# Kernel tuning notes

Hardware: AMD Instinct MI355X
Metric: run time of the kernel (lower is better)

Reference implementation:

```python
import jax, jax.numpy as jnp
import numpy as np

EPS = 1e-5
POOL_R, POOL_T, SCALE = 5, 7, 0.125  # pool_r, pool_t, 1/pool_stride


def conv_bn_relu(x, W, b, gamma, beta, pad):
    # Conv2d(bias) + BatchNorm2d (training-mode batch stats, biased var) + ReLU
    y = jax.lax.conv_general_dilated(x, W, (1, 1), [(pad, pad), (pad, pad)],
                                     dimension_numbers=('NCHW', 'OIHW', 'NCHW'))
    y = y + b[None, :, None, None]
    mean = y.mean(axis=(0, 2, 3))
    var = y.var(axis=(0, 2, 3))
    y = (y - mean[None, :, None, None]) * jax.lax.rsqrt(var + EPS)[None, :, None, None]
    y = y * gamma[None, :, None, None] + beta[None, :, None, None]
    return jax.nn.relu(y)


def linear_bn_relu(x, W, b, gamma, beta):
    # LinearBlock: Linear + BatchNorm (over batch dim) + ReLU
    y = x @ W.T + b
    mean = y.mean(axis=0)
    var = y.var(axis=0)
    y = (y - mean) * jax.lax.rsqrt(var + EPS) * gamma + beta
    return jax.nn.relu(y)


def _hat_int(x):
    # Antiderivative of the triangular (bilinear) hat kernel at offset x.
    u = jnp.clip(x, -1.0, 1.0)
    return jnp.where(u <= 0, 0.5 * (1.0 + u) ** 2, 0.5 + u - 0.5 * u ** 2)


def prroi_pool(feat, rois, ph, pw, scale):
    # Exact PrRoIPool2D. feat: [B,C,H,W]; rois: [B,N,4] xyxy in image coords.
    # Bilinear interp is a sum of separable hat kernels at integer grid points, so the
    # exact bin integral factorizes into per-axis hat-integral weights Wx, Wy.
    B, C, H, W = feat.shape
    x1, y1, x2, y2 = [rois[..., i] * scale for i in range(4)]
    bw = (x2 - x1) / pw   # [B,N]
    bh = (y2 - y1) / ph
    qx = jnp.arange(pw, dtype=feat.dtype)
    qy = jnp.arange(ph, dtype=feat.dtype)
    xs_lo = x1[..., None] + qx * bw[..., None]   # [B,N,Pw]
    ys_lo = y1[..., None] + qy * bh[..., None]   # [B,N,Ph]
    gw = jnp.arange(W, dtype=feat.dtype)
    gh = jnp.arange(H, dtype=feat.dtype)
    Wx = _hat_int(xs_lo[..., None] + bw[..., None, None] - gw) - _hat_int(xs_lo[..., None] - gw)  # [B,N,Pw,W]
    Wy = _hat_int(ys_lo[..., None] + bh[..., None, None] - gh) - _hat_int(ys_lo[..., None] - gh)  # [B,N,Ph,H]
    out = jnp.einsum('bchw,bnph,bnqw->bncpq', feat, Wy, Wx)
    area = (bw * bh)[:, :, None, None, None]
    return jnp.where(area > 0, out / jnp.maximum(area, 1e-12), 0.0)  # [B,N,C,Ph,Pw]


def _forward(feat1, feat2, bb1, proposals2,
             w_c1r, b_c1r, g_c1r, be_c1r,
             w_c1t, b_c1t, g_c1t, be_c1t,
             w_c2t, b_c2t, g_c2t, be_c2t,
             w_f1r, b_f1r, g_f1r, be_f1r,
             w_f2r, b_f2r, g_f2r, be_f2r,
             w_f1rt, b_f1rt, g_f1rt, be_f1rt,
             w_f2rt, b_f2rt, g_f2rt, be_f2rt,
             w_iou, b_iou):
    S = feat2.shape[0]
    N = proposals2.shape[2]
    # --- get_modulation ---
    c3_r = conv_bn_relu(feat1, w_c1r, b_c1r, g_c1r, be_c1r, 1)
    bb = bb1[0]  # [S,4] xywh -> xyxy
    roi_r = jnp.concatenate([bb[:, :2], bb[:, :2] + bb[:, 2:4]], axis=1)[:, None, :]
    pooled_r = prroi_pool(c3_r, roi_r, POOL_R, POOL_R, SCALE)[:, 0]   # [S,256,5,5]
    m = conv_bn_relu(pooled_r, w_f1r, b_f1r, g_f1r, be_f1r, 0)        # [S,1024,1,1]
    m = conv_bn_relu(m, w_f2r, b_f2r, g_f2r, be_f2r, 0)               # [S,256,1,1]
    modulation = m.reshape(S, -1)                                     # [S,256]
    # --- get_iou_feat ---
    c3_t = conv_bn_relu(conv_bn_relu(feat2, w_c1t, b_c1t, g_c1t, be_c1t, 1),
                        w_c2t, b_c2t, g_c2t, be_c2t, 1)
    # --- predict_iou ---
    c3_t_att = c3_t * modulation[:, :, None, None]
    props = proposals2[0]  # [S,N,4] xywh -> xyxy
    rois_t = jnp.concatenate([props[..., :2], props[..., :2] + props[..., 2:4]], axis=-1)
    pooled_t = prroi_pool(c3_t_att, rois_t, POOL_T, POOL_T, SCALE)    # [S,N,256,7,7]
    x = pooled_t.reshape(S * N, -1)
    x = linear_bn_relu(x, w_f1rt, b_f1rt, g_f1rt, be_f1rt)
    x = linear_bn_relu(x, w_f2rt, b_f2rt, g_f2rt, be_f2rt)
    iou = x @ w_iou.T + b_iou
    return iou.reshape(1, S, N)  # (num_images, num_sequences, num_proposals)


def setup_inputs() -> dict:
    key = jax.random.key(0)
    ks = jax.random.split(key, 8)
    S, C, Hf, Wf, N = 64, 256, 36, 36, 16
    inp = {}
    inp['feat1'] = jax.random.normal(ks[0], (S, C, Hf, Wf), jnp.float32)
    inp['feat2'] = jax.random.normal(ks[1], (S, C, Hf, Wf), jnp.float32)
    xy1 = jax.random.uniform(ks[2], (1, S, 2), minval=20.0, maxval=180.0)
    wh1 = jax.random.uniform(ks[3], (1, S, 2), minval=40.0, maxval=100.0)
    inp['bb1'] = jnp.concatenate([xy1, wh1], axis=-1).astype(jnp.float32)
    xy2 = jax.random.uniform(ks[4], (1, S, N, 2), minval=20.0, maxval=180.0)
    wh2 = jax.random.uniform(ks[5], (1, S, N, 2), minval=40.0, maxval=100.0)
    inp['proposals2'] = jnp.concatenate([xy2, wh2], axis=-1).astype(jnp.float32)

    def kaiming(k, shape):
        fan_in = int(np.prod(shape[1:]))
        return (jax.random.normal(k, shape) * np.sqrt(2.0 / fan_in)).astype(jnp.float32)

    kp = jax.random.split(ks[6], 8)
    specs = [('c1r', (256, C, 3, 3), kp[0]), ('c1t', (256, C, 3, 3), kp[1]),
             ('c2t', (256, 256, 3, 3), kp[2]), ('f1r', (1024, 256, 5, 5), kp[3]),
             ('f2r', (256, 1024, 1, 1), kp[4]), ('f1rt', (1024, 256 * 7 * 7), kp[5]),
             ('f2rt', (1024, 1024), kp[6])]
    for name, shape, k in specs:
        inp['w_' + name] = kaiming(k, shape)
        oc = shape[0]
        inp['b_' + name] = jnp.zeros(oc, jnp.float32)
        inp['g_' + name] = jnp.ones(oc, jnp.float32)
        inp['be_' + name] = jnp.zeros(oc, jnp.float32)
    inp['w_iou'] = kaiming(kp[7], (1, 1024))
    inp['b_iou'] = jnp.zeros(1, jnp.float32)
    return inp


def reference(feat1, feat2, bb1, proposals2,
              w_c1r, b_c1r, g_c1r, be_c1r,
              w_c1t, b_c1t, g_c1t, be_c1t,
              w_c2t, b_c2t, g_c2t, be_c2t,
              w_f1r, b_f1r, g_f1r, be_f1r,
              w_f2r, b_f2r, g_f2r, be_f2r,
              w_f1rt, b_f1rt, g_f1rt, be_f1rt,
              w_f2rt, b_f2rt, g_f2rt, be_f2rt,
              w_iou, b_iou):
    return _forward(feat1, feat2, bb1, proposals2,
                    w_c1r, b_c1r, g_c1r, be_c1r,
                    w_c1t, b_c1t, g_c1t, be_c1t,
                    w_c2t, b_c2t, g_c2t, be_c2t,
                    w_f1r, b_f1r, g_f1r, be_f1r,
                    w_f2r, b_f2r, g_f2r, be_f2r,
                    w_f1rt, b_f1rt, g_f1rt, be_f1rt,
                    w_f2rt, b_f2rt, g_f2rt, be_f2rt,
                    w_iou, b_iou)
```

## Files before the change

### kernel.cpp

```cpp
#include <hip/hip_runtime.h>
#include <cstddef>


typedef _Float16 f16;
typedef __attribute__((ext_vector_type(8))) _Float16 f16x8;
typedef __attribute__((ext_vector_type(4))) float f32x4;

__device__ __forceinline__ void gload16(const void* g, void* l) {
  __builtin_amdgcn_global_load_lds((const __attribute__((address_space(1))) void*)g,
                                   (__attribute__((address_space(3))) void*)l, 16, 0, 0);
}

#define WAITB(N) asm volatile("s_waitcnt vmcnt(" #N ")\n\ts_barrier" ::: "memory")
#define LGKB()   asm volatile("s_waitcnt lgkmcnt(0)\n\ts_barrier" ::: "memory")

static __device__ __forceinline__ float hat_int(float x) {
  float u = fminf(1.f, fmaxf(-1.f, x));
  float a = 0.5f * (1.f + u) * (1.f + u);
  float b = 0.5f + u - 0.5f * u * u;
  return (u <= 0.f) ? a : b;
}

static __device__ __forceinline__ size_t pk_off(int row, int k, int K) {
  return (size_t)(row >> 7) * ((size_t)K * 128) + (size_t)(k >> 5) * 4096
       + (size_t)((((k >> 3) & 3) * 128 + (row & 127)) * 8 + (k & 7));
}

__global__ __launch_bounds__(256) void k_padT(const float* __restrict__ src,
                                              f16* __restrict__ FT) {
  __shared__ f16 sT[8][1300];
  const int img = blockIdx.x, kk = blockIdx.y;
  const float* sp = src + ((size_t)img * 256 + kk * 8) * 1296;
#pragma unroll
  for (int c = 0; c < 8; ++c)
    for (int i = threadIdx.x; i < 1296; i += 256)
      sT[c][i] = (f16)sp[c * 1296 + i];
  __syncthreads();
  f16* op = FT + ((size_t)img * 32 + kk) * 1444 * 8;
  for (int i = threadIdx.x; i < 148; i += 256) {
    int r, cc;
    if (i < 38)       { r = 0;          cc = i; }
    else if (i < 76)  { r = 37;         cc = i - 38; }
    else if (i < 112) { r = i - 76 + 1; cc = 0; }
    else              { r = i - 112 + 1; cc = 37; }
    f16x8 z = {};
    *reinterpret_cast<f16x8*>(op + (r * 38 + cc) * 8) = z;
  }
  for (int i = threadIdx.x; i < 1296; i += 256) {
    const int h = i / 36, w = i - h * 36;
    f16x8 v;
#pragma unroll
    for (int c = 0; c < 8; ++c) v[c] = sT[c][i];
    *reinterpret_cast<f16x8*>(op + ((h + 1) * 38 + w + 1) * 8) = v;
  }
}

__global__ void k_pad2(const f16* __restrict__ yH, f16* __restrict__ FT,
                       const float* __restrict__ mean, const float* __restrict__ istd,
                       const float* __restrict__ g, const float* __restrict__ be) {
  const int img = blockIdx.x, h = blockIdx.y, c = threadIdx.x;
  const float sc = istd[c] * g[c];
  const float sh = be[c] - mean[c] * sc;
  const f16* sp = yH + ((size_t)img * 1296 + h * 36) * 256 + c;
  f16* op = FT + (((size_t)img * 32 + (c >> 3)) * 1444 + (h + 1) * 38 + 1) * 8 + (c & 7);
#pragma unroll 4
  for (int w = 0; w < 36; ++w) {
    float v = fmaxf(fmaf((float)sp[w * 256], sc, sh), 0.f);
    op[w * 8] = (f16)v;
  }
}

__global__ void k_pack_wc(const float* __restrict__ w, f16* __restrict__ dst) {
  int i = blockIdx.x * 256 + threadIdx.x;
  int oct = i / 294912;
  int r = i - oct * 294912;
  int ks = r >> 12;
  int r2 = r & 4095;
  int koct = r2 >> 10;
  int r3 = r2 & 1023;
  int row = r3 >> 3, kj = r3 & 7;
  int k = ks * 32 + koct * 8 + kj;
  int t = k >> 8, c = k & 255;
  int oc = oct * 128 + row;
  dst[i] = (f16)w[(oc * 256 + c) * 9 + t];
}

__global__ __launch_bounds__(256) void k_packx_h(
    const f16* __restrict__ src, f16* __restrict__ dst, int M, int K) {
  __shared__ f16 sT[128][264];
  const int k0 = blockIdx.x * 256, r0 = blockIdx.y * 128;
  const int t = threadIdx.x;
  const int rl = t >> 5, kk = (t & 31) * 8;
  for (int rnd = 0; rnd < 16; ++rnd) {
    const int row_l = rl + rnd * 8;
    const int row = r0 + row_l;
    if (row < M) {
      f16x8 v = *reinterpret_cast<const f16x8*>(src + (size_t)row * K + k0 + kk);
      *reinterpret_cast<f16x8*>(&sT[row_l][kk]) = v;
    }
  }
  __syncthreads();
  const size_t base = (size_t)(r0 >> 7) * ((size_t)K * 128) + (size_t)(k0 >> 5) * 4096;
#pragma unroll
  for (int cs = 0; cs < 8; ++cs) {
#pragma unroll
    for (int half = 0; half < 2; ++half) {
      const int e = half * 256 + t;
      const int koct = e >> 7, row_l = e & 127;
      f16x8 v = {};
      if (r0 + row_l < M)
        v = *reinterpret_cast<const f16x8*>(&sT[row_l][cs * 32 + koct * 8]);
      *reinterpret_cast<f16x8*>(dst + base + (size_t)cs * 4096 + e * 8) = v;
    }
  }
}

__global__ __launch_bounds__(256) void k_packx_f(
    const float* __restrict__ src, f16* __restrict__ dst, int M, int K) {
  __shared__ f16 sT[128][264];
  const int k0 = blockIdx.x * 256, r0 = blockIdx.y * 128;
  const int t = threadIdx.x;
  const int rl = t >> 5, kk = (t & 31) * 8;
  for (int rnd = 0; rnd < 16; ++rnd) {
    const int row_l = rl + rnd * 8;
    const int row = r0 + row_l;
    if (row < M) {
      const float4* sp = reinterpret_cast<const float4*>(src + (size_t)row * K + k0 + kk);
      float4 a = sp[0], b = sp[1];
      f16* o = &sT[row_l][kk];
      o[0] = (f16)a.x; o[1] = (f16)a.y; o[2] = (f16)a.z; o[3] = (f16)a.w;
      o[4] = (f16)b.x; o[5] = (f16)b.y; o[6] = (f16)b.z; o[7] = (f16)b.w;
    }
  }
  __syncthreads();
  const size_t base = (size_t)(r0 >> 7) * ((size_t)K * 128) + (size_t)(k0 >> 5) * 4096;
#pragma unroll
  for (int cs = 0; cs < 8; ++cs) {
#pragma unroll
    for (int half = 0; half < 2; ++half) {
      const int e = half * 256 + t;
      const int koct = e >> 7, row_l = e & 127;
      f16x8 v = {};
      if (r0 + row_l < M)
        v = *reinterpret_cast<const f16x8*>(&sT[row_l][cs * 32 + koct * 8]);
      *reinterpret_cast<f16x8*>(dst + base + (size_t)cs * 4096 + e * 8) = v;
    }
  }
}

__global__ __launch_bounds__(256) void k_conv_mfma(
    const f16* __restrict__ Wpk, const f16* __restrict__ FT2,
    const float* __restrict__ bias, f16* __restrict__ yH,
    float* __restrict__ psc) {
  __shared__ __align__(16) char smem[49152];
  f16x8* sA = (f16x8*)smem;
  f16x8* sB = (f16x8*)(smem + 24576);
  const int bid = blockIdx.x;
  const int orig = (bid & 7) * 176 + (bid >> 3);
  const int img = orig / 22;
  const int rem = orig - img * 22;
  const int oct = rem / 11;
  const int pt  = rem - oct * 11;
  const int m0 = oct * 128;
  const int p0 = pt * 128;
  const int tid = threadIdx.x;
  const int lane = tid & 63;
  const int wv = tid >> 6;
  const int wr = wv >> 1, wc = wv & 1;

  const f16* aBase = Wpk + (size_t)oct * 294912 + wv * 1024 + lane * 8;
  const f16* ftImg = FT2 + (size_t)img * 32 * 1444 * 8;
  int pos0 = p0 + lane;
  int pc0 = min(pos0, 1295);
  int pc1 = min(pos0 + 64, 1295);
  int pb0 = (pc0 / 36) * 38 + (pc0 % 36);
  int pb1 = (pc1 / 36) * 38 + (pc1 % 36);

  const int loff = wv * 2048 + lane * 16;

  auto stage = [&](int buf, int ks) {
    const int t = ks >> 3;
    const int dy = t / 3, dx = t - dy * 3;
    const int cs = ks & 7;
    const int dyx = dy * 38 + dx;
    char* lA = (char*)sA + buf * 8192 + loff;
    char* lB = (char*)sB + buf * 8192 + loff;
    const f16* ap = aBase + (size_t)ks * 4096;
    const f16* bp = ftImg + ((size_t)(cs * 4 + wv) * 1444 + dyx) * 8;
    gload16(ap, lA);
    gload16(ap + 512, lA + 1024);
    gload16(bp + pb0 * 8, lB);
    gload16(bp + pb1 * 8, lB + 1024);
  };

  f32x4 acc[4][4] = {};
  const int fidxA = ((lane >> 4) << 7) + wr * 64 + (lane & 15);
  const int fidxB = ((lane >> 4) << 7) + wc * 64 + (lane & 15);

  stage(0, 0); stage(1, 1); stage(2, 2);
  int cur = 0;
  for (int ks = 0; ks < 72; ++ks) {
    const int r = 71 - ks;
    if (r >= 2)      WAITB(8);
    else if (r == 1) WAITB(4);
    else             WAITB(0);
    const int base = cur * 512;
    f16x8 af[4], bf[4];
#pragma unroll
    for (int i = 0; i < 4; ++i) {
      af[i] = sA[base + fidxA + i * 16];
      bf[i] = sB[base + fidxB + i * 16];
    }
    __builtin_amdgcn_s_setprio(1);
#pragma unroll
    for (int i = 0; i < 4; ++i)
#pragma unroll
      for (int j = 0; j < 4; ++j)
        acc[i][j] = __builtin_amdgcn_mfma_f32_16x16x32_f16(af[i], bf[j], acc[i][j], 0, 0, 0);
    __builtin_amdgcn_s_setprio(0);
    LGKB();
    if (ks + 3 < 72) stage(cur, ks + 3);
    cur = (cur == 2) ? 0 : cur + 1;
  }

  __syncthreads();
  f16* sE = (f16*)smem;
  const int ocl = wr * 64 + ((lane >> 4) << 2);
#pragma unroll
  for (int i = 0; i < 4; ++i) {
    const int oc0 = m0 + ocl + i * 16;
    float b0 = bias[oc0], b1 = bias[oc0 + 1], b2 = bias[oc0 + 2], b3 = bias[oc0 + 3];
#pragma unroll
    for (int j = 0; j < 4; ++j) {
      f16* e = &sE[(wc * 64 + j * 16 + (lane & 15)) * 136 + ocl + i * 16];
      e[0] = (f16)(acc[i][j][0] + b0);
      e[1] = (f16)(acc[i][j][1] + b1);
      e[2] = (f16)(acc[i][j][2] + b2);
      e[3] = (f16)(acc[i][j][3] + b3);
    }
  }
  __syncthreads();
  f16* yb = yH + (size_t)img * 1296 * 256 + m0;
#pragma unroll
  for (int it = 0; it < 8; ++it) {
    const int e = (it * 256 + tid) * 8;
    const int row = e >> 7;
    const int oc = e & 127;
    const int col = p0 + row;
    if (col < 1296)
      *reinterpret_cast<f16x8*>(yb + (size_t)col * 256 + oc) =
        *reinterpret_cast<const f16x8*>(&sE[row * 136 + oc]);
  }
  const int nvalid = min(128, 1296 - p0);
  const int half = tid >> 7, cc = tid & 127;
  const int r0 = half * 64, r1 = min(nvalid, r0 + 64);
  float s = 0.f, ss = 0.f;
  for (int row = r0; row < r1; ++row) {
    float v = (float)sE[row * 136 + cc];
    s += v; ss += v * v;
  }
  const int bi = (half * 704 + img * 11 + pt) * 256 + m0 + cc;
  psc[bi] = s;
  psc[360448 + bi] = ss;
}

__global__ void k_chan_fold8(const float* __restrict__ psc, float* __restrict__ out2) {
  const int z = blockIdx.x, c = threadIdx.x;
  float s = 0.f, ss = 0.f;
  for (int i = z * 176; i < z * 176 + 176; ++i) {
    s += psc[i * 256 + c];
    ss += psc[360448 + i * 256 + c];
  }
  out2[z * 256 + c] = s;
  out2[2048 + z * 256 + c] = ss;
}

__global__ void k_chan_final2(const float* __restrict__ out2,
                              float* __restrict__ mean, float* __restrict__ istd) {
  const int c = threadIdx.x;
  float s = 0.f, ss = 0.f;
#pragma unroll
  for (int z = 0; z < 8; ++z) { s += out2[z * 256 + c]; ss += out2[2048 + z * 256 + c]; }
  float m = s * (1.f / 82944.f);
  float var = ss * (1.f / 82944.f) - m * m;
  mean[c] = m;
  istd[c] = rsqrtf(var + 1e-5f);
}

__global__ __launch_bounds__(256) void k_gemm_f16pk(
    const f16* __restrict__ Apk, const f16* __restrict__ Bpk,
    float* __restrict__ part, int K, int Nout, int stepsPerZ, int mrows) {
  __shared__ f16x8 sA[1536];
  __shared__ f16x8 sB[1536];
  const int nt = blockIdx.x, mt = blockIdx.y, z = blockIdx.z;
  const int tid = threadIdx.x;
  const int lane = tid & 63;
  const int wv = tid >> 6;
  const int wr = wv >> 1, wc = wv & 1;

  const f16* aC = Apk + (size_t)mt * K * 128 + wv * 1024 + lane * 8;
  const f16* bC = Bpk + (size_t)nt * K * 128 + wv * 1024 + lane * 8;
  const int loff = wv * 2048 + lane * 16;

  auto stage = [&](int buf, int ks) {
    char* lA = (char*)sA + buf * 8192 + loff;
    char* lB = (char*)sB + buf * 8192 + loff;
    const f16* ap = aC + (size_t)ks * 4096;
    const f16* bp = bC + (size_t)ks * 4096;
    gload16(ap, lA);
    gload16(ap + 512, lA + 1024);
    gload16(bp, lB);
    gload16(bp + 512, lB + 1024);
  };

  f32x4 acc[4][4] = {};
  const int fidxA = ((lane >> 4) << 7) + wr * 64 + (lane & 15);
  const int fidxB = ((lane >> 4) << 7) + wc * 64 + (lane & 15);

  const int ks0 = z * stepsPerZ;
  stage(0, ks0); stage(1, ks0 + 1); stage(2, ks0 + 2);
  int cur = 0;
  for (int i = 0; i < stepsPerZ; ++i) {
    const int r = stepsPerZ - 1 - i;
    if (r >= 2)      WAITB(8);
    else if (r == 1) WAITB(4);
    else             WAITB(0);
    const int base = cur * 512;
    f16x8 af[4], bf[4];
#pragma unroll
    for (int j = 0; j < 4; ++j) {
      af[j] = sA[base + fidxA + j * 16];
      bf[j] = sB[base + fidxB + j * 16];
    }
    __builtin_amdgcn_s_setprio(1);
#pragma unroll
    for (int ii = 0; ii < 4; ++ii)
#pragma unroll
      for (int jj = 0; jj < 4; ++jj)
        acc[ii][jj] = __builtin_amdgcn_mfma_f32_16x16x32_f16(af[ii], bf[jj], acc[ii][jj], 0, 0, 0);
    __builtin_amdgcn_s_setprio(0);
    LGKB();
    if (i + 3 < stepsPerZ) stage(cur, ks0 + i + 3);
    cur = (cur == 2) ? 0 : cur + 1;
  }

  const size_t zoff = (size_t)z * mrows * Nout;
  const int colb = nt * 128 + wc * 64 + (lane & 15);
  const int rowb = mt * 128 + wr * 64 + ((lane >> 4) << 2);
#pragma unroll
  for (int i = 0; i < 4; ++i)
#pragma unroll
    for (int j = 0; j < 4; ++j)
#pragma unroll
      for (int r = 0; r < 4; ++r)
        part[zoff + (size_t)(rowb + i * 16 + r) * Nout + colb + j * 16] = acc[i][j][r];
}

__global__ void k_reduce_stats(const float* __restrict__ part, const float* __restrict__ bias,
                               float* __restrict__ out, int mrows, int Mout, int Nout,
                               int sk, int rpz,
                               float* __restrict__ psum, float* __restrict__ psq) {
  const int col = blockIdx.x * 256 + threadIdx.x;
  const int z = blockIdx.y;
  const float b = bias[col];
  float s = 0.f, ss = 0.f;
  const int r0 = z * rpz, r1 = min(Mout, r0 + rpz);
  for (int m = r0; m < r1; ++m) {
    float v = b;
    for (int zz = 0; zz < sk; ++zz)
      v += part[(size_t)zz * mrows * Nout + (size_t)m * Nout + col];
    out[(size_t)m * Nout + col] = v;
    s += v; ss += v * v;
  }
  psum[(size_t)z * Nout + col] = s;
  psq[(size_t)z * Nout + col] = ss;
}

__global__ void k_wxy(const float* __restrict__ rois, int ntot, int P,
                      float* __restrict__ Wx, float* __restrict__ Wy,
                      float* __restrict__ area,
                      int* __restrict__ HLO, int* __restrict__ HCNT,
                      int* __restrict__ WLO) {
  int idx = blockIdx.x * blockDim.x + threadIdx.x;
  if (idx >= ntot) return;
  float rx = rois[idx * 4 + 0], ry = rois[idx * 4 + 1];
  float rw = rois[idx * 4 + 2], rh = rois[idx * 4 + 3];
  float x1 = rx * 0.125f, y1 = ry * 0.125f;
  float x2 = (rx + rw) * 0.125f, y2 = (ry + rh) * 0.125f;
  float bw = (x2 - x1) / P, bh = (y2 - y1) / P;
  area[idx] = bw * bh;
  int hlo = max(0, (int)ceilf(y1 - 1.f));
  int hhi = min(35, (int)floorf(y2 + 1.f));
  HLO[idx] = hlo;
  HCNT[idx] = max(0, hhi - hlo + 1);
  for (int q = 0; q < P; ++q) {
    float xlo = x1 + q * bw, ylo = y1 + q * bh;
    WLO[idx * P + q] = min(31, max(0, (int)ceilf(xlo - 1.f)));
    for (int g = 0; g < 36; ++g) {
      float fg = (float)g;
      Wx[(idx * P + q) * 36 + g] = hat_int(xlo + bw - fg) - hat_int(xlo - fg);
      Wy[(idx * P + q) * 36 + g] = hat_int(ylo + bh - fg) - hat_int(ylo - fg);
    }
  }
}

template <int P, bool MOD>
__global__ __launch_bounds__(256) void k_pool(
    const f16* __restrict__ feat, const float* __restrict__ Wx,
    const float* __restrict__ Wy, const float* __restrict__ area,
    const int* __restrict__ HLO, const int* __restrict__ HCNT,
    const int* __restrict__ WLO,
    const float* __restrict__ mean, const float* __restrict__ istd,
    const float* __restrict__ g, const float* __restrict__ be,
    const float* __restrict__ mod, f16* __restrict__ out, int N) {
  const int s = blockIdx.x, n = blockIdx.y;
  const int idx = s * N + n;
  const int c = threadIdx.x;
  constexpr int KD = P * P * 256;
  __shared__ f16 sOut[KD];
  __shared__ float sWx[P * 36], sWy[P * 36];
  __shared__ int sWLO[P];
  __shared__ int sH[2];
  for (int i = threadIdx.x; i < P * 36; i += 256) {
    sWx[i] = Wx[(size_t)idx * P * 36 + i];
    sWy[i] = Wy[(size_t)idx * P * 36 + i];
  }
  if (threadIdx.x < P) sWLO[threadIdx.x] = WLO[idx * P + threadIdx.x];
  if (threadIdx.x == 0) { sH[0] = HLO[idx]; sH[1] = HCNT[idx]; }
  __syncthreads();
  const float sc = istd[c] * g[c];
  const float sh = be[c] - mean[c] * sc;
  const f16* f = feat + (size_t)s * 1296 * 256 + c;
  float o[P][P] = {};
  const int hlo = sH[0], hcnt = sH[1];
  for (int hh = 0; hh < hcnt; ++hh) {
    const int h = hlo + hh;
    const f16* rp = f + (size_t)h * 36 * 256;
    float colsum[P];
#pragma unroll
    for (int q = 0; q < P; ++q) {
      const int w0 = sWLO[q];
      const f16* wp = rp + (size_t)w0 * 256;
      float v = 0.f;
#pragma unroll
      for (int j = 0; j < 5; ++j) {
        float x = fmaxf(fmaf((float)wp[j * 256], sc, sh), 0.f);
        v = fmaf(sWx[q * 36 + w0 + j], x, v);
      }
      colsum[q] = v;
    }
#pragma unroll
    for (int p = 0; p < P; ++p) {
      const float wy = sWy[p * 36 + h];
      if (wy != 0.f) {
#pragma unroll
        for (int q = 0; q < P; ++q) o[p][q] = fmaf(wy, colsum[q], o[p][q]);
      }
    }
  }
  float a = area[idx];
  float inv = (a > 0.f) ? 1.f / fmaxf(a, 1e-12f) : 0.f;
  float msc = MOD ? (mod[s * 256 + c] * inv) : inv;
  const int kbase = c * (P * P);
#pragma unroll
  for (int p = 0; p < P; ++p)
#pragma unroll
    for (int q = 0; q < P; ++q)
      sOut[kbase + p * P + q] = (f16)(o[p][q] * msc);
  __syncthreads();
  f16* op = out + (size_t)idx * KD;
  for (int j = threadIdx.x; j < KD; j += 256) op[j] = sOut[j];
}

__global__ void k_fc_stats_final(const float* __restrict__ psum, const float* __restrict__ psq,
                                 int nz, int Nf, int M,
                                 float* __restrict__ mean, float* __restrict__ istd) {
  int col = blockIdx.x * 256 + threadIdx.x;
  if (col >= Nf) return;
  float s = 0.f, ss = 0.f;
  for (int z = 0; z < nz; ++z) {
    s += psum[(size_t)z * Nf + col];
    ss += psq[(size_t)z * Nf + col];
  }
  float mu = s / (float)M;
  float var = ss / (float)M - mu * mu;
  mean[col] = mu;
  istd[col] = rsqrtf(var + 1e-5f);
}

__global__ void k_fc_bn_relu(float* __restrict__ y, const float* __restrict__ mean,
                             const float* __restrict__ istd, const float* __restrict__ g,
                             const float* __restrict__ be, int total, int Nf) {
  int i = blockIdx.x * 256 + threadIdx.x;
  if (i >= total) return;
  int col = i % Nf;
  float sc = istd[col] * g[col];
  float sh = be[col] - mean[col] * sc;
  y[i] = fmaxf(fmaf(y[i], sc, sh), 0.f);
}

__global__ void k_fc_bn_relu_pk(const float* __restrict__ y, const float* __restrict__ mean,
                                const float* __restrict__ istd, const float* __restrict__ g,
                                const float* __restrict__ be, f16* __restrict__ xpk,
                                int total, int Nf) {
  int i = blockIdx.x * 256 + threadIdx.x;
  if (i >= total) return;
  int row = i / Nf, col = i - row * Nf;
  float sc = istd[col] * g[col];
  float sh = be[col] - mean[col] * sc;
  float v = fmaxf(fmaf(y[i], sc, sh), 0.f);
  xpk[pk_off(row, col, Nf)] = (f16)v;
}

__global__ void k_zero(float4* __restrict__ p, int n4) {
  int i = blockIdx.x * 256 + threadIdx.x;
  if (i < n4) p[i] = float4{0.f, 0.f, 0.f, 0.f};
}

__global__ void k_iou(const float* __restrict__ x, const float* __restrict__ w,
                      const float* __restrict__ b, float* __restrict__ out) {
  const int r = blockIdx.x, tid = threadIdx.x;
  float s = 0.f;
  for (int k = tid; k < 1024; k += 256) s = fmaf(x[(size_t)r * 1024 + k], w[k], s);
  __shared__ float red[256];
  red[tid] = s;
  __syncthreads();
  for (int o = 128; o > 0; o >>= 1) {
    if (tid < o) red[tid] += red[tid + o];
    __syncthreads();
  }
  if (tid == 0) out[r] = red[0] + b[0];
}

static const size_t O_A      = 0;
static const size_t O_POOLT  = 12000000;
static const size_t O_PSC2   = 12000000;
static const size_t O_PSC2B  = 12800000;
static const size_t O_PSUM   = 13000000;
static const size_t O_PSQ    = 13200000;
static const size_t O_WPK2RT = 16000000;
static const size_t O_POOLR  = 18500000;
static const size_t O_WPK2R  = 20000000;
static const size_t O_FT     = 21233664;
static const size_t O_X2PK   = 21233664 + 6422528;
static const size_t O_WC     = 33062912;
static const size_t O_WPK1RT = 33357824;
static const size_t O_WPK1R  = 39780352;
static const size_t O_PRPK   = 43057152;
static const size_t O_Y1     = 43466752;
static const size_t O_Y2     = 44515328;
static const size_t O_MOD    = 45563904;
static const size_t O_WXR    = 45580288;
static const size_t O_WYR    = 45591808;
static const size_t O_ARR    = 45603328;
static const size_t O_WXT    = 45603392;
static const size_t O_WYT    = 45861440;
static const size_t O_ART    = 46119488;
static const size_t O_MEAN   = 46120512;
static const size_t O_ISTD   = 46121536;
static const size_t O_X1PK   = 46122560;
static const size_t O_META   = 46188096;

extern "C" void kernel_launch(void* const* d_in, const int* in_sizes, int n_in,
                              void* d_out, int out_size, void* d_ws, size_t ws_size,
                              hipStream_t stream) {
  (void)in_sizes; (void)n_in; (void)out_size; (void)ws_size;
  const float* feat1  = (const float*)d_in[0];
  const float* feat2  = (const float*)d_in[1];
  const float* bb1    = (const float*)d_in[2];
  const float* props  = (const float*)d_in[3];
  const float* w_c1r  = (const float*)d_in[4];
  const float* b_c1r  = (const float*)d_in[5];
  const float* g_c1r  = (const float*)d_in[6];
  const float* be_c1r = (const float*)d_in[7];
  const float* w_c1t  = (const float*)d_in[8];
  const float* b_c1t  = (const float*)d_in[9];
  const float* g_c1t  = (const float*)d_in[10];
  const float* be_c1t = (const float*)d_in[11];
  const float* w_c2t  = (const float*)d_in[12];
  const float* b_c2t  = (const float*)d_in[13];
  const float* g_c2t  = (const float*)d_in[14];
  const float* be_c2t = (const float*)d_in[15];
  const float* w_f1r  = (const float*)d_in[16];
  const float* b_f1r  = (const float*)d_in[17];
  const float* g_f1r  = (const float*)d_in[18];
  const float* be_f1r = (const float*)d_in[19];
  const float* w_f2r  = (const float*)d_in[20];
  const float* b_f2r  = (const float*)d_in[21];
  const float* g_f2r  = (const float*)d_in[22];
  const float* be_f2r = (const float*)d_in[23];
  const float* w_f1rt = (const float*)d_in[24];
  const float* b_f1rt = (const float*)d_in[25];
  const float* g_f1rt = (const float*)d_in[26];
  const float* be_f1rt= (const float*)d_in[27];
  const float* w_f2rt = (const float*)d_in[28];
  const float* b_f2rt = (const float*)d_in[29];
  const float* g_f2rt = (const float*)d_in[30];
  const float* be_f2rt= (const float*)d_in[31];
  const float* w_iou  = (const float*)d_in[32];
  const float* b_iou  = (const float*)d_in[33];

  float* ws    = (float*)d_ws;
  f16*   AH    = (f16*)(ws + O_A);
  float* PART  = ws + O_A;
  f16*   POOLT = (f16*)(ws + O_POOLT);
  float* PSC2  = ws + O_PSC2;
  float* PSC2B = ws + O_PSC2B;
  float* PSUM  = ws + O_PSUM;
  float* PSQ   = ws + O_PSQ;
  f16*   WPK2RT= (f16*)(ws + O_WPK2RT);
  f16*   POOLR = (f16*)(ws + O_POOLR);
  f16*   WPK2R = (f16*)(ws + O_WPK2R);
  f16*   FT2   = (f16*)(ws + O_FT);
  f16*   PHPK  = FT2;
  f16*   X2PK  = (f16*)(ws + O_X2PK);
  f16*   WC    = (f16*)(ws + O_WC);
  f16*   WPK1RT= (f16*)(ws + O_WPK1RT);
  f16*   WPK1R = (f16*)(ws + O_WPK1R);
  f16*   PRPK  = (f16*)(ws + O_PRPK);
  float* Y1    = ws + O_Y1;
  float* Y2    = ws + O_Y2;
  float* MODp  = ws + O_MOD;
  float* WXR   = ws + O_WXR;
  float* WYR   = ws + O_WYR;
  float* ARR   = ws + O_ARR;
  float* WXT   = ws + O_WXT;
  float* WYT   = ws + O_WYT;
  float* ART   = ws + O_ART;
  float* MEAN  = ws + O_MEAN;
  float* ISTD  = ws + O_ISTD;
  f16*   X1PK  = (f16*)(ws + O_X1PK);
  int*   META  = (int*)(ws + O_META);
  int* HLOR = META;
  int* HCNTR= META + 64;
  int* WLOR = META + 128;
  int* HLOT = META + 448;
  int* HCNTT= META + 1472;
  int* WLOT = META + 2496;

  k_pack_wc<<<2304, 256, 0, stream>>>(w_c1r, WC);
  k_padT<<<dim3(64, 32), 256, 0, stream>>>(feat1, FT2);
  k_conv_mfma<<<1408, 256, 0, stream>>>(WC, FT2, b_c1r, AH, PSC2);
  k_chan_fold8<<<8, 256, 0, stream>>>(PSC2, PSC2B);
  k_chan_final2<<<1, 256, 0, stream>>>(PSC2B, MEAN, ISTD);

  k_wxy<<<1, 64, 0, stream>>>(bb1, 64, 5, WXR, WYR, ARR, HLOR, HCNTR, WLOR);
  k_pool<5, false><<<dim3(64, 1), 256, 0, stream>>>(
      AH, WXR, WYR, ARR, HLOR, HCNTR, WLOR, MEAN, ISTD, g_c1r, be_c1r, nullptr, POOLR, 1);
  k_packx_h<<<dim3(25, 1), 256, 0, stream>>>(POOLR, PRPK, 64, 6400);

  k_packx_f<<<dim3(25, 8), 256, 0, stream>>>(w_f1r, WPK1R, 1024, 6400);
  k_gemm_f16pk<<<dim3(8, 1, 8), 256, 0, stream>>>(PRPK, WPK1R, PART, 6400, 1024, 25, 128);
  k_reduce_stats<<<dim3(4, 8), 256, 0, stream>>>(PART, b_f1r, Y1, 128, 64, 1024, 8, 8, PSUM, PSQ);
  k_fc_stats_final<<<4, 256, 0, stream>>>(PSUM, PSQ, 8, 1024, 64, MEAN, ISTD);
  k_zero<<<64, 256, 0, stream>>>((float4*)X1PK, 16384);
  k_fc_bn_relu_pk<<<256, 256, 0, stream>>>(Y1, MEAN, ISTD, g_f1r, be_f1r, X1PK, 64 * 1024, 1024);

  k_packx_f<<<dim3(4, 2), 256, 0, stream>>>(w_f2r, WPK2R, 256, 1024);
  k_gemm_f16pk<<<dim3(2, 1, 4), 256, 0, stream>>>(X1PK, WPK2R, PART, 1024, 256, 8, 128);
  k_reduce_stats<<<dim3(1, 8), 256, 0, stream>>>(PART, b_f2r, MODp, 128, 64, 256, 4, 8, PSUM, PSQ);
  k_fc_stats_final<<<1, 256, 0, stream>>>(PSUM, PSQ, 8, 256, 64, MEAN, ISTD);
  k_fc_bn_relu<<<64, 256, 0, stream>>>(MODp, MEAN, ISTD, g_f2r, be_f2r, 64 * 256, 256);

  k_pack_wc<<<2304, 256, 0, stream>>>(w_c1t, WC);
  k_padT<<<dim3(64, 32), 256, 0, stream>>>(feat2, FT2);
  k_conv_mfma<<<1408, 256, 0, stream>>>(WC, FT2, b_c1t, AH, PSC2);
  k_chan_fold8<<<8, 256, 0, stream>>>(PSC2, PSC2B);
  k_chan_final2<<<1, 256, 0, stream>>>(PSC2B, MEAN, ISTD);
  k_pad2<<<dim3(64, 36), 256, 0, stream>>>(AH, FT2, MEAN, ISTD, g_c1t, be_c1t);

  k_pack_wc<<<2304, 256, 0, stream>>>(w_c2t, WC);
  k_conv_mfma<<<1408, 256, 0, stream>>>(WC, FT2, b_c2t, AH, PSC2);
  k_chan_fold8<<<8, 256, 0, stream>>>(PSC2, PSC2B);
  k_chan_final2<<<1, 256, 0, stream>>>(PSC2B, MEAN, ISTD);

  k_wxy<<<16, 64, 0, stream>>>(props, 1024, 7, WXT, WYT, ART, HLOT, HCNTT, WLOT);
  k_pool<7, true><<<dim3(64, 16), 256, 0, stream>>>(
      AH, WXT, WYT, ART, HLOT, HCNTT, WLOT, MEAN, ISTD, g_c2t, be_c2t, MODp, POOLT, 16);
  k_packx_h<<<dim3(49, 8), 256, 0, stream>>>(POOLT, PHPK, 1024, 12544);

  k_packx_f<<<dim3(49, 8), 256, 0, stream>>>(w_f1rt, WPK1RT, 1024, 12544);
  k_gemm_f16pk<<<dim3(8, 8, 8), 256, 0, stream>>>(PHPK, WPK1RT, PART, 12544, 1024, 49, 1024);
  k_reduce_stats<<<dim3(4, 128), 256, 0, stream>>>(PART, b_f1rt, Y1, 1024, 1024, 1024, 8, 8, PSUM, PSQ);
  k_fc_stats_final<<<4, 256, 0, stream>>>(PSUM, PSQ, 128, 1024, 1024, MEAN, ISTD);
  k_fc_bn_relu_pk<<<4096, 256, 0, stream>>>(Y1, MEAN, ISTD, g_f1rt, be_f1rt, X2PK, 1024 * 1024, 1024);

  k_packx_f<<<dim3(4, 8), 256, 0, stream>>>(w_f2rt, WPK2RT, 1024, 1024);
  k_gemm_f16pk<<<dim3(8, 8, 4), 256, 0, stream>>>(X2PK, WPK2RT, PART, 1024, 1024, 8, 1024);
  k_reduce_stats<<<dim3(4, 128), 256, 0, stream>>>(PART, b_f2rt, Y2, 1024, 1024, 1024, 4, 8, PSUM, PSQ);
  k_fc_stats_final<<<4, 256, 0, stream>>>(PSUM, PSQ, 128, 1024, 1024, MEAN, ISTD);
  k_fc_bn_relu<<<4096, 256, 0, stream>>>(Y2, MEAN, ISTD, g_f2rt, be_f2rt, 1024 * 1024, 1024);

  k_iou<<<1024, 256, 0, stream>>>(Y2, w_iou, b_iou, (float*)d_out);
}
```

Baseline: 900.3 us.

## Load conv weight fragments directly into registers and fuse zero-padding into BN pack

The conv MFMA kernel stops staging weight (A) tiles through LDS. Each wave now loads its A fragments straight into registers with global_load_dwordx4, triple-buffered alongside the LDS B stages, which shrinks shared memory and adds a launch bound of 2 blocks per SU for higher occupancy. The k_zero launch is removed: the BN/ReLU pack kernel now writes zeros for padding rows past Mvalid itself. This trades LDS traffic and barrier pressure for more VGPRs and redundant global loads of A across the waves that share a row group.

```diff
diff --git a/kernel.cpp b/kernel.cpp
--- a/kernel.cpp
+++ b/kernel.cpp
@@ -9,6 +9,12 @@
 __device__ __forceinline__ void gload16(const void* g, void* l) {
   __builtin_amdgcn_global_load_lds((const __attribute__((address_space(1))) void*)g,
                                    (__attribute__((address_space(3))) void*)l, 16, 0, 0);
+}
+
+__device__ __forceinline__ f16x8 gload_reg(const f16* p) {
+  f16x8 v;
+  asm volatile("global_load_dwordx4 %0, %1, off" : "=&v"(v) : "v"(p) : "memory");
+  return v;
 }
 
 #define WAITB(N) asm volatile("s_waitcnt vmcnt(" #N ")\n\ts_barrier" ::: "memory")
@@ -148,13 +154,12 @@
   }
 }
 
-__global__ __launch_bounds__(256) void k_conv_mfma(
+__global__ __launch_bounds__(256, 2) void k_conv_mfma(
     const f16* __restrict__ Wpk, const f16* __restrict__ FT2,
     const float* __restrict__ bias, f16* __restrict__ yH,
     float* __restrict__ psc) {
-  __shared__ __align__(16) char smem[49152];
-  f16x8* sA = (f16x8*)smem;
-  f16x8* sB = (f16x8*)(smem + 24576);
+  __shared__ __align__(16) char smem[36864];
+  f16x8* sB = (f16x8*)smem;
   const int bid = blockIdx.x;
   const int orig = (bid & 7) * 176 + (bid >> 3);
   const int img = orig / 22;
@@ -168,7 +173,8 @@
   const int wv = tid >> 6;
   const int wr = wv >> 1, wc = wv & 1;
 
-  const f16* aBase = Wpk + (size_t)oct * 294912 + wv * 1024 + lane * 8;
+  const f16* aFrag = Wpk + (size_t)oct * 294912 + ((lane >> 4) << 10)
+                   + ((size_t)(wr * 64 + (lane & 15)) << 3);
   const f16* ftImg = FT2 + (size_t)img * 32 * 1444 * 8;
   int pos0 = p0 + lane;
   int pc0 = min(pos0, 1295);
@@ -178,50 +184,60 @@
 
   const int loff = wv * 2048 + lane * 16;
 
-  auto stage = [&](int buf, int ks) {
+  auto stageB = [&](int buf, int ks) {
     const int t = ks >> 3;
     const int dy = t / 3, dx = t - dy * 3;
     const int cs = ks & 7;
     const int dyx = dy * 38 + dx;
-    char* lA = (char*)sA + buf * 8192 + loff;
     char* lB = (char*)sB + buf * 8192 + loff;
-    const f16* ap = aBase + (size_t)ks * 4096;
     const f16* bp = ftImg + ((size_t)(cs * 4 + wv) * 1444 + dyx) * 8;
-    gload16(ap, lA);
-    gload16(ap + 512, lA + 1024);
     gload16(bp + pb0 * 8, lB);
     gload16(bp + pb1 * 8, lB + 1024);
   };
 
+#define LOADA(ASET, KS)                                                        \
+  {                                                                            \
+    const f16* _p = aFrag + (size_t)(KS) * 4096;                               \
+    ASET[0] = gload_reg(_p);                                                   \
+    ASET[1] = gload_reg(_p + 128);                                             \
+    ASET[2] = gload_reg(_p + 256);                                             \
+    ASET[3] = gload_reg(_p + 384);                                             \
+  }
+
   f32x4 acc[4][4] = {};
-  const int fidxA = ((lane >> 4) << 7) + wr * 64 + (lane & 15);
   const int fidxB = ((lane >> 4) << 7) + wc * 64 + (lane & 15);
-
-  stage(0, 0); stage(1, 1); stage(2, 2);
-  int cur = 0;
-  for (int ks = 0; ks < 72; ++ks) {
-    const int r = 71 - ks;
-    if (r >= 2)      WAITB(8);
-    else if (r == 1) WAITB(4);
-    else             WAITB(0);
-    const int base = cur * 512;
-    f16x8 af[4], bf[4];
-#pragma unroll
-    for (int i = 0; i < 4; ++i) {
-      af[i] = sA[base + fidxA + i * 16];
-      bf[i] = sB[base + fidxB + i * 16];
-    }
-    __builtin_amdgcn_s_setprio(1);
-#pragma unroll
-    for (int i = 0; i < 4; ++i)
-#pragma unroll
-      for (int j = 0; j < 4; ++j)
-        acc[i][j] = __builtin_amdgcn_mfma_f32_16x16x32_f16(af[i], bf[j], acc[i][j], 0, 0, 0);
-    __builtin_amdgcn_s_setprio(0);
-    LGKB();
-    if (ks + 3 < 72) stage(cur, ks + 3);
-    cur = (cur == 2) ? 0 : cur + 1;
-  }
+  f16x8 A0[4], A1[4], A2[4];
+
+  stageB(0, 0); LOADA(A0, 0);
+  stageB(1, 1); LOADA(A1, 1);
+  stageB(2, 2); LOADA(A2, 2);
+
+#define CSTEP(ASET, BUF, KS)                                                   \
+  {                                                                            \
+    const int rr = 71 - (KS);                                                  \
+    if (rr >= 2)      WAITB(12);                                               \
+    else if (rr == 1) WAITB(6);                                                \
+    else              WAITB(0);                                                \
+    __builtin_amdgcn_sched_barrier(0);                                         \
+    f16x8 bf[4];                                                               \
+    _Pragma("unroll") for (int j = 0; j < 4; ++j)                              \
+      bf[j] = sB[(BUF) * 512 + fidxB + j * 16];                                \
+    __builtin_amdgcn_s_setprio(1);                                             \
+    _Pragma("unroll") for (int ii = 0; ii < 4; ++ii)                           \
+      _Pragma("unroll") for (int jj = 0; jj < 4; ++jj)                         \
+        acc[ii][jj] = __builtin_amdgcn_mfma_f32_16x16x32_f16(ASET[ii], bf[jj], acc[ii][jj], 0, 0, 0); \
+    __builtin_amdgcn_s_setprio(0);                                             \
+    LGKB();                                                                    \
+    if ((KS) + 3 < 72) { stageB(BUF, (KS) + 3); LOADA(ASET, (KS) + 3); }       \
+  }
+
+  for (int ks = 0; ks < 72; ks += 3) {
+    CSTEP(A0, 0, ks);
+    CSTEP(A1, 1, ks + 1);
+    CSTEP(A2, 2, ks + 2);
+  }
+#undef CSTEP
+#undef LOADA
 
   __syncthreads();
   f16* sE = (f16*)smem;
@@ -502,19 +518,17 @@
 __global__ void k_fc_bn_relu_pk(const float* __restrict__ y, const float* __restrict__ mean,
                                 const float* __restrict__ istd, const float* __restrict__ g,
                                 const float* __restrict__ be, f16* __restrict__ xpk,
-                                int total, int Nf) {
+                                int total, int Nf, int Mvalid) {
   int i = blockIdx.x * 256 + threadIdx.x;
   if (i >= total) return;
   int row = i / Nf, col = i - row * Nf;
-  float sc = istd[col] * g[col];
-  float sh = be[col] - mean[col] * sc;
-  float v = fmaxf(fmaf(y[i], sc, sh), 0.f);
+  float v = 0.f;
+  if (row < Mvalid) {
+    float sc = istd[col] * g[col];
+    float sh = be[col] - mean[col] * sc;
+    v = fmaxf(fmaf(y[i], sc, sh), 0.f);
+  }
   xpk[pk_off(row, col, Nf)] = (f16)v;
-}
-
-__global__ void k_zero(float4* __restrict__ p, int n4) {
-  int i = blockIdx.x * 256 + threadIdx.x;
-  if (i < n4) p[i] = float4{0.f, 0.f, 0.f, 0.f};
 }
 
 __global__ void k_iou(const float* __restrict__ x, const float* __restrict__ w,
@@ -653,8 +667,7 @@
   k_gemm_f16pk<<<dim3(8, 1, 8), 256, 0, stream>>>(PRPK, WPK1R, PART, 6400, 1024, 25, 128);
   k_reduce_stats<<<dim3(4, 8), 256, 0, stream>>>(PART, b_f1r, Y1, 128, 64, 1024, 8, 8, PSUM, PSQ);
   k_fc_stats_final<<<4, 256, 0, stream>>>(PSUM, PSQ, 8, 1024, 64, MEAN, ISTD);
-  k_zero<<<64, 256, 0, stream>>>((float4*)X1PK, 16384);
-  k_fc_bn_relu_pk<<<256, 256, 0, stream>>>(Y1, MEAN, ISTD, g_f1r, be_f1r, X1PK, 64 * 1024, 1024);
+  k_fc_bn_relu_pk<<<512, 256, 0, stream>>>(Y1, MEAN, ISTD, g_f1r, be_f1r, X1PK, 128 * 1024, 1024, 64);
 
   k_packx_f<<<dim3(4, 2), 256, 0, stream>>>(w_f2r, WPK2R, 256, 1024);
   k_gemm_f16pk<<<dim3(2, 1, 4), 256, 0, stream>>>(X1PK, WPK2R, PART, 1024, 256, 8, 128);
@@ -683,7 +696,7 @@
   k_gemm_f16pk<<<dim3(8, 8, 8), 256, 0, stream>>>(PHPK, WPK1RT, PART, 12544, 1024, 49, 1024);
   k_reduce_stats<<<dim3(4, 128), 256, 0, stream>>>(PART, b_f1rt, Y1, 1024, 1024, 1024, 8, 8, PSUM, PSQ);
   k_fc_stats_final<<<4, 256, 0, stream>>>(PSUM, PSQ, 128, 1024, 1024, MEAN, ISTD);
-  k_fc_bn_relu_pk<<<4096, 256, 0, stream>>>(Y1, MEAN, ISTD, g_f1rt, be_f1rt, X2PK, 1024 * 1024, 1024);
+  k_fc_bn_relu_pk<<<4096, 256, 0, stream>>>(Y1, MEAN, ISTD, g_f1rt, be_f1rt, X2PK, 1024 * 1024, 1024, 1024);
 
   k_packx_f<<<dim3(4, 8), 256, 0, stream>>>(w_f2rt, WPK2RT, 1024, 1024);
   k_gemm_f16pk<<<dim3(8, 8, 4), 256, 0, stream>>>(X2PK, WPK2RT, PART, 1024, 1024, 8, 1024);
```

New measurement: 899.4 us. No clear change (-0.1%).
